# Optimization experiments

Hardware: AMD Instinct MI355X
Metric: run time of the kernel (lower is better)

## Reference

```python
import jax, jax.numpy as jnp
import numpy as np

EPS = 1e-5

def setup_inputs() -> dict:
    key = jax.random.key(0)
    ks = jax.random.split(key, 4)
    B, F, H, W = 32, 2048, 7, 7
    hw = H * W
    A = 1
    return {
        "x": jax.random.normal(ks[0], (B, F, H, W), dtype=jnp.float32),
        "W_qkv": jax.random.normal(ks[1], (3 * hw, hw), dtype=jnp.float32) * (hw ** -0.5),
        "W_out": jax.random.normal(ks[2], (A, hw), dtype=jnp.float32) * (hw ** -0.5),
        "b_out": jax.random.normal(ks[3], (A,), dtype=jnp.float32) * 0.01,
        "gamma": jnp.ones((F,), dtype=jnp.float32),
        "beta": jnp.zeros((F,), dtype=jnp.float32),
    }

def reference(x, W_qkv, W_out, b_out, gamma, beta):
    B, F, H, W = x.shape
    hw = H * W
    scale = hw ** -0.5
    xf = x.reshape(B, F, hw)                       # [B, F, 49]
    qkv = jnp.einsum("bfd,ed->bfe", xf, W_qkv)   # [B, F, 147]
    q, k, v = jnp.split(qkv, 3, axis=-1)           # each [B, F, 49]
    scores = jnp.einsum("bfd,bgd->bfg", q, k) * scale   # [B, F, F]
    probs = jax.nn.softmax(scores, axis=-1)
    attn_out = jnp.einsum("bfg,bgd->bfd", probs, v)      # [B, F, 49]
    out = jnp.einsum("bfd,ad->bfa", attn_out, W_out) + b_out  # [B, F, A]
    # BatchNorm1d (training mode): per-channel (axis=1) stats over (batch, length)
    mean = out.mean(axis=(0, 2), keepdims=True)
    var = out.var(axis=(0, 2), keepdims=True)  # biased variance, as torch uses for normalization
    out = (out - mean) * jax.lax.rsqrt(var + EPS)
    return out * gamma[None, :, None] + beta[None, :, None]
```

## Files before the change

### kernel.cpp

```cpp
#include <hip/hip_runtime.h>
#include <math.h>

#define BB    32
#define FF    2048
#define HW    49
#define ROWS  (BB * FF)
#define DPAD  64
#define SPLIT 4
#define GHALF (FF / SPLIT)
#define NST   (GHALF / 32)
#define HNST  (NST / 2)

typedef float f32x16 __attribute__((ext_vector_type(16)));
typedef _Float16 f16x8 __attribute__((ext_vector_type(8)));
typedef short s16x8 __attribute__((ext_vector_type(8)));

__device__ inline float exp2_fast(float x) {
    return __builtin_amdgcn_exp2f(x);
}

__device__ inline unsigned f16pack(float v) {
    _Float16 h = (_Float16)v;
    _Float16 l = (_Float16)(v - (float)h);
    unsigned hb = (unsigned)__builtin_bit_cast(unsigned short, h);
    unsigned lb = (unsigned)__builtin_bit_cast(unsigned short, l);
    return (hb << 16) | lb;
}

__device__ inline void unpack8(uint4 a, uint4 b, f16x8& h, f16x8& l) {
    unsigned w[8] = {a.x, a.y, a.z, a.w, b.x, b.y, b.z, b.w};
    s16x8 hs, ls;
    #pragma unroll
    for (int i = 0; i < 8; ++i) {
        hs[i] = (short)(w[i] >> 16);
        ls[i] = (short)(w[i] & 0xFFFFu);
    }
    h = __builtin_bit_cast(f16x8, hs);
    l = __builtin_bit_cast(f16x8, ls);
}

__global__ __launch_bounds__(256) void prep_kernel(
    const float* __restrict__ Wqkv, const float* __restrict__ Wout,
    unsigned* __restrict__ Mtpk, float* __restrict__ u)
{
    __shared__ float W2[98][52];
    const int tid = threadIdx.x;
    if (blockIdx.x < 16) {
        for (int i = tid; i < 98 * 52; i += 256) {
            int e = i / 52, j = i - e * 52;
            W2[e][j] = (j < HW) ? Wqkv[e * HW + j] : 0.f;
        }
        __syncthreads();
        const int d = blockIdx.x * 4 + (tid >> 6);
        const int j = tid & 63;
        float s = 0.f;
        if (d < HW && j < HW) {
            for (int e = 0; e < HW; ++e) s = fmaf(W2[e][j], W2[49 + e][d], s);
            s *= 0.2060992915555662f;
        }
        Mtpk[d * 64 + j] = f16pack(s);
    } else {
        if (tid < 64) {
            float s = 0.f;
            if (tid < HW)
                for (int e = 0; e < HW; ++e)
                    s = fmaf(Wqkv[(98 + e) * HW + tid], Wout[e], s);
            u[tid] = s;
        }
    }
}

__global__ __launch_bounds__(128) void xy_kernel(
    const float* __restrict__ x, const float* __restrict__ u,
    const unsigned* __restrict__ Mtpk,
    unsigned short* __restrict__ xf, unsigned short* __restrict__ yh,
    float* __restrict__ wv)
{
    __shared__ float xsh[64 * HW];
    __shared__ float ush[64];
    const int blk = (blockIdx.x & 7) * 128 + (blockIdx.x >> 3);
    const int tid = threadIdx.x, lane = tid & 63, wid = tid >> 6;
    const int col = lane & 31, half = lane >> 5;
    if (tid < 64) ush[tid] = u[tid];

    {
        const float* xb = x + (size_t)blk * 64 * HW;
        for (int i = tid; i < 64 * HW; i += 128) xsh[i] = xb[i];
    }
    __syncthreads();

    const int r0 = blk * 64 + wid * 32;
    const int rloc = wid * 32 + col;
    const int row = r0 + col;
    const int tile = blk * 2 + wid;

    f16x8 ah[4], al[4];
    float wp = 0.f;
    #pragma unroll
    for (int ks = 0; ks < 4; ++ks) {
        s16x8 hs, ls;
        #pragma unroll
        for (int i = 0; i < 8; ++i) {
            int d = ks * 16 + half * 8 + i;
            float t = (d < HW) ? xsh[rloc * HW + d] : 0.f;
            wp = fmaf(t, ush[d], wp);
            _Float16 h = (_Float16)t;
            _Float16 l = (_Float16)(t - (float)h);
            hs[i] = __builtin_bit_cast(short, h);
            ls[i] = __builtin_bit_cast(short, l);
        }
        ah[ks] = __builtin_bit_cast(f16x8, hs);
        al[ks] = __builtin_bit_cast(f16x8, ls);
        *(f16x8*)(xf + ((size_t)tile * 4 + ks) * 512 + lane * 8) = ah[ks];
    }
    wp += __shfl_xor(wp, 32);
    if (half == 0) wv[row] = wp;

    for (int dt = 0; dt < 2; ++dt) {
        f16x8 mh[4], ml[4];
        #pragma unroll
        for (int ks = 0; ks < 4; ++ks) {
            const unsigned* mp = Mtpk + (dt * 32 + col) * 64 + ks * 16 + half * 8;
            unpack8(*(const uint4*)mp, *(const uint4*)(mp + 4), mh[ks], ml[ks]);
        }
        f32x16 acc;
        #pragma unroll
        for (int i = 0; i < 16; ++i) acc[i] = 0.f;
        #pragma unroll
        for (int ks = 0; ks < 4; ++ks) {
            acc = __builtin_amdgcn_mfma_f32_32x32x16_f16(ah[ks], ml[ks], acc, 0, 0, 0);
            acc = __builtin_amdgcn_mfma_f32_32x32x16_f16(al[ks], mh[ks], acc, 0, 0, 0);
            acc = __builtin_amdgcn_mfma_f32_32x32x16_f16(ah[ks], mh[ks], acc, 0, 0, 0);
        }
        #pragma unroll
        for (int reg = 0; reg < 16; ++reg) {
            int drow = (reg & 3) + 8 * (reg >> 2) + 4 * half;
            _Float16 hv = (_Float16)acc[reg];
            yh[(size_t)(r0 + drow) * DPAD + dt * 32 + col] =
                __builtin_bit_cast(unsigned short, hv);
        }
    }
}

__global__ __launch_bounds__(256, 4) void attn_kernel(
    const unsigned short* __restrict__ xf, const unsigned short* __restrict__ yh,
    const float* __restrict__ wv,
    float* __restrict__ partL, float* __restrict__ partA)
{
    const int bid = blockIdx.x;
    const int L = (bid & 7) * 256 + (bid >> 3);
    const int b   = L >> 6;
    const int r63 = L & 63;

    const int tid  = threadIdx.x;
    const int lane = tid & 63;
    const int wid  = tid >> 6;
    const int col  = lane & 31;
    const int half = lane >> 5;

    const int sp  = r63 >> 4;
    const int ftg = (r63 & 15) * 4 + wid;
    const int fblk0  = ftg * 32;
    const int gstart = sp * GHALF;
    const size_t bq = (size_t)b * FF;

    f16x8 qhf[4];
    {
        const size_t yrow = (bq + fblk0 + col) * DPAD;
        #pragma unroll
        for (int ks = 0; ks < 4; ++ks)
            qhf[ks] = *(const f16x8*)(yh + yrow + ks * 16 + half * 8);
    }

    const unsigned short* abase =
        xf + ((size_t)(b * (FF / 32) + sp * NST) * 4) * 512 + lane * 8;
    const float* wbase = wv + bq + gstart + 4 * half;

    float lsum = 0.f;
    float a0 = 0.f, a1 = 0.f, a2 = 0.f, a3 = 0.f;

    #pragma unroll
    for (int j = 0; j < HNST; ++j) {
        f16x8 af0[4], af1[4];
        #pragma unroll
        for (int ks = 0; ks < 4; ++ks)
            af0[ks] = *(const f16x8*)(abase + (size_t)j * 2048 + ks * 512);
        #pragma unroll
        for (int ks = 0; ks < 4; ++ks)
            af1[ks] = *(const f16x8*)(abase + (size_t)(j + HNST) * 2048 + ks * 512);

        f32x16 acc0, acc1;
        #pragma unroll
        for (int i = 0; i < 16; ++i) { acc0[i] = 0.f; acc1[i] = 0.f; }
        #pragma unroll
        for (int ks = 0; ks < 4; ++ks)
            acc0 = __builtin_amdgcn_mfma_f32_32x32x16_f16(af0[ks], qhf[ks], acc0, 0, 0, 0);
        #pragma unroll
        for (int ks = 0; ks < 4; ++ks)
            acc1 = __builtin_amdgcn_mfma_f32_32x32x16_f16(af1[ks], qhf[ks], acc1, 0, 0, 0);

        const float* wpb0 = wbase + j * 32;
        #pragma unroll
        for (int q = 0; q < 4; ++q) {
            float4 w4 = *(const float4*)(wpb0 + q * 8);
            float p0 = exp2_fast(acc0[q * 4 + 0]);
            float p1 = exp2_fast(acc0[q * 4 + 1]);
            float p2 = exp2_fast(acc0[q * 4 + 2]);
            float p3 = exp2_fast(acc0[q * 4 + 3]);
            lsum += ((p0 + p1) + (p2 + p3));
            a0 = fmaf(p0, w4.x, a0);
            a1 = fmaf(p1, w4.y, a1);
            a2 = fmaf(p2, w4.z, a2);
            a3 = fmaf(p3, w4.w, a3);
        }
        const float* wpb1 = wbase + (j + HNST) * 32;
        #pragma unroll
        for (int q = 0; q < 4; ++q) {
            float4 w4 = *(const float4*)(wpb1 + q * 8);
            float p0 = exp2_fast(acc1[q * 4 + 0]);
            float p1 = exp2_fast(acc1[q * 4 + 1]);
            float p2 = exp2_fast(acc1[q * 4 + 2]);
            float p3 = exp2_fast(acc1[q * 4 + 3]);
            lsum += ((p0 + p1) + (p2 + p3));
            a0 = fmaf(p0, w4.x, a0);
            a1 = fmaf(p1, w4.y, a1);
            a2 = fmaf(p2, w4.z, a2);
            a3 = fmaf(p3, w4.w, a3);
        }
    }

    float asum = (a0 + a1) + (a2 + a3);
    lsum += __shfl_xor(lsum, 32);
    asum += __shfl_xor(asum, 32);
    if (half == 0) {
        size_t o = ((size_t)sp * BB + b) * FF + fblk0 + col;
        partL[o] = lsum;
        partA[o] = asum;
    }
}

__global__ __launch_bounds__(64) void bn_kernel(
    const float* __restrict__ partL, const float* __restrict__ partA,
    const float* __restrict__ gamma, const float* __restrict__ beta,
    float* __restrict__ out)
{
    const int f = blockIdx.x * 64 + threadIdx.x;
    float v[BB];
    float mean = 0.f;
    #pragma unroll
    for (int b = 0; b < BB; ++b) {
        float l = 0.f, a = 0.f;
        #pragma unroll
        for (int s = 0; s < SPLIT; ++s) {
            l += partL[((size_t)s * BB + b) * FF + f];
            a += partA[((size_t)s * BB + b) * FF + f];
        }
        v[b] = a / l;
        mean += v[b];
    }
    mean *= (1.f / BB);
    float var = 0.f;
    #pragma unroll
    for (int b = 0; b < BB; ++b) {
        float d = v[b] - mean;
        var = fmaf(d, d, var);
    }
    var *= (1.f / BB);
    const float inv = rsqrtf(var + 1e-5f);
    const float g = gamma[f], be = beta[f];
    #pragma unroll
    for (int b = 0; b < BB; ++b)
        out[((size_t)b << 11) + f] = (v[b] - mean) * inv * g + be;
}

extern "C" void kernel_launch(void* const* d_in, const int* in_sizes, int n_in,
                              void* d_out, int out_size, void* d_ws, size_t ws_size,
                              hipStream_t stream)
{
    const float* x     = (const float*)d_in[0];
    const float* Wqkv  = (const float*)d_in[1];
    const float* Wout  = (const float*)d_in[2];
    const float* gamma = (const float*)d_in[4];
    const float* beta  = (const float*)d_in[5];

    char* wsb = (char*)d_ws;
    const size_t PANEL = (size_t)ROWS * DPAD * sizeof(unsigned short);
    unsigned short* xf = (unsigned short*)(wsb);
    unsigned short* yh = (unsigned short*)(wsb + PANEL);
    float*          wv = (float*)(wsb + 2 * PANEL);
    unsigned*     Mtpk = (unsigned*)(wsb + 2 * PANEL + 262144);
    float*           u = (float*)(wsb + 2 * PANEL + 262144 + 16384);
    float*       partL = (float*)(wsb + 2 * PANEL + 262144 + 17408);
    float*       partA = partL + (size_t)SPLIT * BB * FF;

    prep_kernel<<<dim3(17), dim3(256), 0, stream>>>(Wqkv, Wout, Mtpk, u);

    xy_kernel<<<dim3(ROWS / 64), dim3(128), 0, stream>>>(
        x, u, Mtpk, xf, yh, wv);

    attn_kernel<<<dim3(BB * 64), dim3(256), 0, stream>>>(
        xf, yh, wv, partL, partA);

    bn_kernel<<<dim3(FF / 64), dim3(64), 0, stream>>>(
        partL, partA, gamma, beta, (float*)d_out);
}
```

Baseline: 71.80 us.

## Switch attention scores to 16x16x32 MFMA tiles with double-buffered key loads

The attention kernel now computes score tiles with 16x16x32 f16 MFMA instead of 32x32x16, so each wave owns 16 query rows and twice as many blocks are launched. The xy kernel writes the key panel in a layout matched to the new 16-row fragment format. The inner loop prefetches the next key tile into a second register buffer while the current one is processed. The aim is higher occupancy and a smaller accumulator register footprint, plus memory latency hidden behind the exp/accumulate work. The cost is that each key tile is read by twice as many waves, and an extra cross-lane shuffle is needed for the final reduction.

```diff
diff --git a/kernel.cpp b/kernel.cpp
--- a/kernel.cpp
+++ b/kernel.cpp
@@ -8,9 +8,9 @@
 #define DPAD  64
 #define SPLIT 4
 #define GHALF (FF / SPLIT)
-#define NST   (GHALF / 32)
-#define HNST  (NST / 2)
-
+#define NT16  (GHALF / 16)
+
+typedef float f32x4 __attribute__((ext_vector_type(4)));
 typedef float f32x16 __attribute__((ext_vector_type(16)));
 typedef _Float16 f16x8 __attribute__((ext_vector_type(8)));
 typedef short s16x8 __attribute__((ext_vector_type(8)));
@@ -92,7 +92,7 @@
     const int r0 = blk * 64 + wid * 32;
     const int rloc = wid * 32 + col;
     const int row = r0 + col;
-    const int tile = blk * 2 + wid;
+    const int tile16 = row >> 4;
 
     f16x8 ah[4], al[4];
     float wp = 0.f;
@@ -111,7 +111,10 @@
         }
         ah[ks] = __builtin_bit_cast(f16x8, hs);
         al[ks] = __builtin_bit_cast(f16x8, ls);
-        *(f16x8*)(xf + ((size_t)tile * 4 + ks) * 512 + lane * 8) = ah[ks];
+        const int c = 2 * ks + half;
+        const int kf = c >> 2;
+        const int lp = (row & 15) | ((c & 3) << 4);
+        *(f16x8*)(xf + ((size_t)tile16 * 2 + kf) * 512 + lp * 8) = ah[ks];
     }
     wp += __shfl_xor(wp, 32);
     if (half == 0) wv[row] = wp;
@@ -148,79 +151,79 @@
     float* __restrict__ partL, float* __restrict__ partA)
 {
     const int bid = blockIdx.x;
-    const int L = (bid & 7) * 256 + (bid >> 3);
-    const int b   = L >> 6;
-    const int r63 = L & 63;
+    const int L = (bid & 7) * 512 + (bid >> 3);
+    const int b    = L >> 7;
+    const int r127 = L & 127;
 
     const int tid  = threadIdx.x;
     const int lane = tid & 63;
     const int wid  = tid >> 6;
-    const int col  = lane & 31;
-    const int half = lane >> 5;
-
-    const int sp  = r63 >> 4;
-    const int ftg = (r63 & 15) * 4 + wid;
-    const int fblk0  = ftg * 32;
+    const int f16i = lane & 15;
+    const int g4   = lane >> 4;
+
+    const int sp  = r127 >> 5;
+    const int fg  = (r127 & 31) * 4 + wid;
+    const int fblk0  = fg * 16;
     const int gstart = sp * GHALF;
     const size_t bq = (size_t)b * FF;
 
-    f16x8 qhf[4];
+    f16x8 qk[2];
     {
-        const size_t yrow = (bq + fblk0 + col) * DPAD;
-        #pragma unroll
-        for (int ks = 0; ks < 4; ++ks)
-            qhf[ks] = *(const f16x8*)(yh + yrow + ks * 16 + half * 8);
+        const size_t yrow = (bq + fblk0 + f16i) * DPAD;
+        #pragma unroll
+        for (int kf = 0; kf < 2; ++kf)
+            qk[kf] = *(const f16x8*)(yh + yrow + kf * 32 + g4 * 8);
     }
 
     const unsigned short* abase =
-        xf + ((size_t)(b * (FF / 32) + sp * NST) * 4) * 512 + lane * 8;
-    const float* wbase = wv + bq + gstart + 4 * half;
+        xf + ((size_t)(b * (FF / 16) + sp * NT16) * 2) * 512 + lane * 8;
+    const float* wbase = wv + bq + gstart + g4 * 4;
 
     float lsum = 0.f;
     float a0 = 0.f, a1 = 0.f, a2 = 0.f, a3 = 0.f;
 
-    #pragma unroll
-    for (int j = 0; j < HNST; ++j) {
-        f16x8 af0[4], af1[4];
-        #pragma unroll
-        for (int ks = 0; ks < 4; ++ks)
-            af0[ks] = *(const f16x8*)(abase + (size_t)j * 2048 + ks * 512);
-        #pragma unroll
-        for (int ks = 0; ks < 4; ++ks)
-            af1[ks] = *(const f16x8*)(abase + (size_t)(j + HNST) * 2048 + ks * 512);
-
-        f32x16 acc0, acc1;
-        #pragma unroll
-        for (int i = 0; i < 16; ++i) { acc0[i] = 0.f; acc1[i] = 0.f; }
-        #pragma unroll
-        for (int ks = 0; ks < 4; ++ks)
-            acc0 = __builtin_amdgcn_mfma_f32_32x32x16_f16(af0[ks], qhf[ks], acc0, 0, 0, 0);
-        #pragma unroll
-        for (int ks = 0; ks < 4; ++ks)
-            acc1 = __builtin_amdgcn_mfma_f32_32x32x16_f16(af1[ks], qhf[ks], acc1, 0, 0, 0);
-
-        const float* wpb0 = wbase + j * 32;
-        #pragma unroll
-        for (int q = 0; q < 4; ++q) {
-            float4 w4 = *(const float4*)(wpb0 + q * 8);
-            float p0 = exp2_fast(acc0[q * 4 + 0]);
-            float p1 = exp2_fast(acc0[q * 4 + 1]);
-            float p2 = exp2_fast(acc0[q * 4 + 2]);
-            float p3 = exp2_fast(acc0[q * 4 + 3]);
+    f16x8 afA[2], afB[2];
+    #pragma unroll
+    for (int kf = 0; kf < 2; ++kf)
+        afA[kf] = *(const f16x8*)(abase + (size_t)kf * 512);
+
+    #pragma unroll
+    for (int t = 0; t < NT16; t += 2) {
+        #pragma unroll
+        for (int kf = 0; kf < 2; ++kf)
+            afB[kf] = *(const f16x8*)(abase + (size_t)(t + 1) * 1024 + kf * 512);
+
+        {
+            f32x4 acc = {0.f, 0.f, 0.f, 0.f};
+            acc = __builtin_amdgcn_mfma_f32_16x16x32_f16(afA[0], qk[0], acc, 0, 0, 0);
+            acc = __builtin_amdgcn_mfma_f32_16x16x32_f16(afA[1], qk[1], acc, 0, 0, 0);
+            float4 w4 = *(const float4*)(wbase + t * 16);
+            float p0 = exp2_fast(acc[0]);
+            float p1 = exp2_fast(acc[1]);
+            float p2 = exp2_fast(acc[2]);
+            float p3 = exp2_fast(acc[3]);
             lsum += ((p0 + p1) + (p2 + p3));
             a0 = fmaf(p0, w4.x, a0);
             a1 = fmaf(p1, w4.y, a1);
             a2 = fmaf(p2, w4.z, a2);
             a3 = fmaf(p3, w4.w, a3);
         }
-        const float* wpb1 = wbase + (j + HNST) * 32;
-        #pragma unroll
-        for (int q = 0; q < 4; ++q) {
-            float4 w4 = *(const float4*)(wpb1 + q * 8);
-            float p0 = exp2_fast(acc1[q * 4 + 0]);
-            float p1 = exp2_fast(acc1[q * 4 + 1]);
-            float p2 = exp2_fast(acc1[q * 4 + 2]);
-            float p3 = exp2_fast(acc1[q * 4 + 3]);
+
+        if (t + 2 < NT16) {
+            #pragma unroll
+            for (int kf = 0; kf < 2; ++kf)
+                afA[kf] = *(const f16x8*)(abase + (size_t)(t + 2) * 1024 + kf * 512);
+        }
+
+        {
+            f32x4 acc = {0.f, 0.f, 0.f, 0.f};
+            acc = __builtin_amdgcn_mfma_f32_16x16x32_f16(afB[0], qk[0], acc, 0, 0, 0);
+            acc = __builtin_amdgcn_mfma_f32_16x16x32_f16(afB[1], qk[1], acc, 0, 0, 0);
+            float4 w4 = *(const float4*)(wbase + (t + 1) * 16);
+            float p0 = exp2_fast(acc[0]);
+            float p1 = exp2_fast(acc[1]);
+            float p2 = exp2_fast(acc[2]);
+            float p3 = exp2_fast(acc[3]);
             lsum += ((p0 + p1) + (p2 + p3));
             a0 = fmaf(p0, w4.x, a0);
             a1 = fmaf(p1, w4.y, a1);
@@ -230,10 +233,12 @@
     }
 
     float asum = (a0 + a1) + (a2 + a3);
+    lsum += __shfl_xor(lsum, 16);
+    asum += __shfl_xor(asum, 16);
     lsum += __shfl_xor(lsum, 32);
     asum += __shfl_xor(asum, 32);
-    if (half == 0) {
-        size_t o = ((size_t)sp * BB + b) * FF + fblk0 + col;
+    if (g4 == 0) {
+        size_t o = ((size_t)sp * BB + b) * FF + fblk0 + f16i;
         partL[o] = lsum;
         partA[o] = asum;
     }
@@ -298,7 +303,7 @@
     xy_kernel<<<dim3(ROWS / 64), dim3(128), 0, stream>>>(
         x, u, Mtpk, xf, yh, wv);
 
-    attn_kernel<<<dim3(BB * 64), dim3(256), 0, stream>>>(
+    attn_kernel<<<dim3(BB * 128), dim3(256), 0, stream>>>(
         xf, yh, wv, partL, partA);
 
     bn_kernel<<<dim3(FF / 64), dim3(64), 0, stream>>>(
```

Result: slower. 83.99 us (+17.0%).
